# Kernel tuning notes

Measured on AMD Instinct MI355X. Metric: run time of the kernel, lower is better.

The kernel has to match this reference:

```python
import jax, jax.numpy as jnp
import numpy as np


def _gcn_conv(x, W, b, src, dst, dinv):
    # PyG GCNConv: linear transform, then symmetric-normalized aggregation, then bias
    n = x.shape[0]
    h = x @ W  # [N, out]
    norm = (dinv[src] * dinv[dst])[:, None]  # [E, 1]
    msg = h[src] * norm  # gather + scale, [E, out]
    out = jax.ops.segment_sum(msg, dst, num_segments=n)  # scatter-add
    return out + b


def setup_inputs() -> dict:
    key = jax.random.key(0)
    k1, k2, k3, k4 = jax.random.split(key, 4)
    N, E, F_IN, F_HID, F_OUT = 50000, 800000, 512, 256, 64
    x = jax.random.normal(k1, (N, F_IN), dtype=jnp.float32)
    edge_index = jax.random.randint(k2, (2, E), 0, N, dtype=jnp.int64)
    # Glorot-ish init for weights
    W1 = jax.random.normal(k3, (F_IN, F_HID), dtype=jnp.float32) * (1.0 / np.sqrt(F_IN))
    b1 = jnp.zeros((F_HID,), dtype=jnp.float32)
    W2 = jax.random.normal(k4, (F_HID, F_OUT), dtype=jnp.float32) * (1.0 / np.sqrt(F_HID))
    b2 = jnp.zeros((F_OUT,), dtype=jnp.float32)
    return {"x": x, "edge_index": edge_index, "W1": W1, "b1": b1, "W2": W2, "b2": b2}


def reference(x, edge_index, W1, b1, W2, b2):
    n = x.shape[0]
    # Add self loops (GCNConv default)
    loop = jnp.arange(n, dtype=edge_index.dtype)
    src = jnp.concatenate([edge_index[0], loop])
    dst = jnp.concatenate([edge_index[1], loop])
    # Symmetric normalization D^{-1/2} (A+I) D^{-1/2}
    deg = jax.ops.segment_sum(jnp.ones_like(dst, dtype=x.dtype), dst, num_segments=n)
    dinv = jnp.where(deg > 0, jax.lax.rsqrt(deg), 0.0)
    h = _gcn_conv(x, W1, b1, src, dst, dinv)
    h = jax.nn.relu(h)
    # Dropout(p=0.5) is identity in eval mode (deterministic reference)
    h = _gcn_conv(h, W2, b2, src, dst, dinv)
    return jax.nn.log_softmax(h, axis=1)
```

## Files before the change

### kernel.cpp

```cpp
#include <hip/hip_runtime.h>
#include <math.h>

#define F_IN  512
#define F_HID 256
#define F_OUT 64

typedef __attribute__((ext_vector_type(8))) short bf16x8;
typedef __attribute__((ext_vector_type(4))) short bf16x4;
typedef __attribute__((ext_vector_type(4))) float f32x4;

#define GLOBAL_AS __attribute__((address_space(1)))
#define LDS_AS    __attribute__((address_space(3)))

__device__ __forceinline__ void gload_lds16(const ushort* g, ushort* l) {
    __builtin_amdgcn_global_load_lds((const GLOBAL_AS uint32_t*)g,
                                     (LDS_AS uint32_t*)l, 16, 0, 0);
}

__device__ __forceinline__ ushort f2bf(float f) {
    union { float f; uint32_t u; } v; v.f = f;
    uint32_t r = (v.u + 0x7FFFu + ((v.u >> 16) & 1u)) >> 16;
    return (ushort)r;
}

__device__ __forceinline__ float bf2f(ushort u) {
    union { uint32_t u; float f; } v; v.u = ((uint32_t)u) << 16;
    return v.f;
}

__global__ void k_deg(const int* __restrict__ dst, int* __restrict__ deg, int E) {
    int e = blockIdx.x * 256 + threadIdx.x;
    if (e < E) atomicAdd(&deg[dst[e]], 1);
}

__global__ void k_scan1(const int* __restrict__ deg, int* __restrict__ offs,
                        int* __restrict__ bsums, float* __restrict__ dinv, int N) {
    __shared__ int s[256];
    int tid = threadIdx.x;
    int i = blockIdx.x * 256 + tid;
    int v = (i < N) ? deg[i] : 0;
    if (i < N) dinv[i] = rsqrtf((float)(v + 1));
    s[tid] = v; __syncthreads();
    for (int d = 1; d < 256; d <<= 1) {
        int t = (tid >= d) ? s[tid - d] : 0;
        __syncthreads();
        s[tid] += t;
        __syncthreads();
    }
    if (i < N) offs[i] = s[tid] - v;
    if (tid == 255) bsums[blockIdx.x] = s[255];
}

__global__ void k_scan2(int* __restrict__ bsums, int n) {
    __shared__ int s[256];
    int tid = threadIdx.x;
    int v = (tid < n) ? bsums[tid] : 0;
    s[tid] = v; __syncthreads();
    for (int d = 1; d < 256; d <<= 1) {
        int t = (tid >= d) ? s[tid - d] : 0;
        __syncthreads();
        s[tid] += t;
        __syncthreads();
    }
    if (tid < n) bsums[tid] = s[tid] - v;
}

__global__ void k_scan3(int* __restrict__ offs, const int* __restrict__ bsums,
                        int* __restrict__ cursor, int2* __restrict__ jw, int N, int E) {
    int i = blockIdx.x * 256 + threadIdx.x;
    if (i < N) {
        int o = offs[i] + bsums[i >> 8];
        offs[i] = o;
        cursor[i] = o;
    }
    if (i == 0) offs[N] = E;
    if (i < 16) jw[E + i] = make_int2(0, 0);
}

__global__ void k_fill(const int* __restrict__ src, const int* __restrict__ dst,
                       int* __restrict__ cursor, int2* __restrict__ jw,
                       const float* __restrict__ dinv, int E) {
    int e = blockIdx.x * 256 + threadIdx.x;
    if (e < E) {
        int s = src[e];
        int pos = atomicAdd(&cursor[dst[e]], 1);
        jw[pos] = make_int2(s, __float_as_int(dinv[s]));
    }
}

__global__ void k_tcast2(const float* __restrict__ W1, ushort* __restrict__ w1t,
                         const float* __restrict__ W2, ushort* __restrict__ w2t) {
    int idx = blockIdx.x * 256 + threadIdx.x;
    const int n1 = F_IN * F_HID;
    if (idx < n1) {
        int n = idx / F_IN, k = idx - n * F_IN;
        w1t[idx] = f2bf(W1[(size_t)k * F_HID + n]);
    } else {
        int t = idx - n1;
        if (t < F_HID * F_OUT) {
            int n = t / F_HID, k = t - n * F_HID;
            w2t[t] = f2bf(W2[(size_t)k * F_OUT + n]);
        }
    }
}

__global__ __launch_bounds__(256) void k_gemm1(
        const float* __restrict__ A, const ushort* __restrict__ Bt,
        ushort* __restrict__ C, int M) {
    constexpr int K = F_IN, Nc = F_HID, BM = 64, BN = 128, NT = K / 32;
    constexpr int ASTR = 36;
    __shared__ ushort As[2][BM * ASTR];
    __shared__ ushort Bs[2][BN * 32];
    const int tid  = threadIdx.x;
    const int wave = tid >> 6, lane = tid & 63;
    const int wr = wave & 1, wc = wave >> 1;
    const int brow = blockIdx.y * BM, bcol = blockIdx.x * BN;

    f32x4 acc[2][4];
    #pragma unroll
    for (int m = 0; m < 2; ++m)
        #pragma unroll
        for (int n = 0; n < 4; ++n) acc[m][n] = (f32x4){0.f, 0.f, 0.f, 0.f};

    const int arow = tid >> 2;
    const int akc  = (tid & 3) * 8;
    int agrow = brow + arow; if (agrow >= M) agrow = M - 1;
    const float4* ap = (const float4*)&A[(size_t)agrow * K + akc];
    const int csrc = (tid & 3) ^ ((tid >> 3) & 3);
    const ushort* bp0 = &Bt[(size_t)(bcol + (tid >> 2)) * K + csrc * 8];
    const ushort* bp1 = &Bt[(size_t)(bcol + 64 + (tid >> 2)) * K + csrc * 8];

    const int kqA = (lane >> 4) * 8;
    const int kqB = ((lane >> 4) ^ ((lane >> 1) & 3)) * 8;
    const int rA0 = wr * 32 + (lane & 15);
    const int rB0 = wc * 64 + (lane & 15);

    {
        float4 v0 = ap[0], v1 = ap[1];
        bf16x8 c0;
        c0[0] = (short)f2bf(v0.x); c0[1] = (short)f2bf(v0.y);
        c0[2] = (short)f2bf(v0.z); c0[3] = (short)f2bf(v0.w);
        c0[4] = (short)f2bf(v1.x); c0[5] = (short)f2bf(v1.y);
        c0[6] = (short)f2bf(v1.z); c0[7] = (short)f2bf(v1.w);
        *(bf16x8*)&As[0][arow * ASTR + akc] = c0;
        gload_lds16(bp0, &Bs[0][wave * 512]);
        gload_lds16(bp1, &Bs[0][2048 + wave * 512]);
    }
    __syncthreads();

    #pragma unroll
    for (int t = 0; t < NT; ++t) {
        const int b = t & 1;
        if (t + 1 < NT) {
            gload_lds16(bp0 + (t + 1) * 32, &Bs[b ^ 1][wave * 512]);
            gload_lds16(bp1 + (t + 1) * 32, &Bs[b ^ 1][2048 + wave * 512]);
            float4 v0 = ap[(t + 1) * 8], v1 = ap[(t + 1) * 8 + 1];
            bf16x8 c0;
            c0[0] = (short)f2bf(v0.x); c0[1] = (short)f2bf(v0.y);
            c0[2] = (short)f2bf(v0.z); c0[3] = (short)f2bf(v0.w);
            c0[4] = (short)f2bf(v1.x); c0[5] = (short)f2bf(v1.y);
            c0[6] = (short)f2bf(v1.z); c0[7] = (short)f2bf(v1.w);
            *(bf16x8*)&As[b ^ 1][arow * ASTR + akc] = c0;
        }
        bf16x8 af[2], bfr[4];
        #pragma unroll
        for (int m = 0; m < 2; ++m)
            af[m] = *(const bf16x8*)&As[b][(rA0 + m * 16) * ASTR + kqA];
        #pragma unroll
        for (int n = 0; n < 4; ++n)
            bfr[n] = *(const bf16x8*)&Bs[b][(rB0 + n * 16) * 32 + kqB];
        #pragma unroll
        for (int m = 0; m < 2; ++m)
            #pragma unroll
            for (int n = 0; n < 4; ++n)
                acc[m][n] = __builtin_amdgcn_mfma_f32_16x16x32_bf16(af[m], bfr[n], acc[m][n], 0, 0, 0);
        if (t + 1 < NT) __syncthreads();
    }

    const int crow0 = brow + wr * 32 + (lane >> 4) * 4;
    const int ccol0 = bcol + wc * 64 + (lane & 15);
    #pragma unroll
    for (int m = 0; m < 2; ++m)
        #pragma unroll
        for (int n = 0; n < 4; ++n)
            #pragma unroll
            for (int j = 0; j < 4; ++j) {
                int row = crow0 + m * 16 + j;
                if (row < M) C[(size_t)row * Nc + ccol0 + n * 16] = f2bf(acc[m][n][j]);
            }
}

template<int WR, int WC, int MR, int NR>
__global__ __launch_bounds__(256) void k_gemm_bf16(
        const ushort* __restrict__ A, const ushort* __restrict__ Bt,
        ushort* __restrict__ C, int M, int K, int Nc) {
    constexpr int BM = WR * MR * 16;
    constexpr int BN = WC * NR * 16;
    __shared__ ushort As[BM * 32];
    __shared__ ushort Bs[BN * 32];
    const int tid  = threadIdx.x;
    const int wave = tid >> 6, lane = tid & 63;
    const int wr = wave % WR, wc = wave / WR;
    const int brow = blockIdx.y * BM, bcol = blockIdx.x * BN;

    f32x4 acc[MR][NR];
    #pragma unroll
    for (int m = 0; m < MR; ++m)
        #pragma unroll
        for (int n = 0; n < NR; ++n) acc[m][n] = (f32x4){0.f, 0.f, 0.f, 0.f};

    const int srow = tid >> 2;
    const int scol = (tid & 3) * 8;
    const int kq  = (lane >> 4) * 8;
    const int rA0 = wr * MR * 16 + (lane & 15);
    const int rB0 = wc * NR * 16 + (lane & 15);

    for (int k0 = 0; k0 < K; k0 += 32) {
        #pragma unroll
        for (int l = 0; l < BM / 64; ++l) {
            int row = brow + l * 64 + srow;
            if (row >= M) row = M - 1;
            gload_lds16(&A[(size_t)row * K + k0 + scol], &As[l * 2048 + wave * 512]);
        }
        #pragma unroll
        for (int l = 0; l < BN / 64; ++l) {
            int row = bcol + l * 64 + srow;
            gload_lds16(&Bt[(size_t)row * K + k0 + scol], &Bs[l * 2048 + wave * 512]);
        }
        __syncthreads();
        bf16x8 af[MR], bfr[NR];
        #pragma unroll
        for (int m = 0; m < MR; ++m)
            af[m] = *(const bf16x8*)&As[(rA0 + m * 16) * 32 + kq];
        #pragma unroll
        for (int n = 0; n < NR; ++n)
            bfr[n] = *(const bf16x8*)&Bs[(rB0 + n * 16) * 32 + kq];
        #pragma unroll
        for (int m = 0; m < MR; ++m)
            #pragma unroll
            for (int n = 0; n < NR; ++n)
                acc[m][n] = __builtin_amdgcn_mfma_f32_16x16x32_bf16(af[m], bfr[n], acc[m][n], 0, 0, 0);
        __syncthreads();
    }

    const int crow0 = brow + wr * MR * 16 + (lane >> 4) * 4;
    const int ccol0 = bcol + wc * NR * 16 + (lane & 15);
    #pragma unroll
    for (int m = 0; m < MR; ++m)
        #pragma unroll
        for (int n = 0; n < NR; ++n)
            #pragma unroll
            for (int j = 0; j < 4; ++j) {
                int row = crow0 + m * 16 + j;
                if (row < M) C[(size_t)row * Nc + ccol0 + n * 16] = f2bf(acc[m][n][j]);
            }
}

__global__ __launch_bounds__(256) void k_agg1(
        const ushort* __restrict__ h, const int2* __restrict__ jw,
        const int* __restrict__ offs, const float* __restrict__ dinv,
        const float* __restrict__ bias, ushort* __restrict__ outm, int N) {
    int wave = threadIdx.x >> 6, lane = threadIdx.x & 63;
    int i = blockIdx.x * 4 + wave;
    if (i >= N) return;
    int g = lane & 31;
    int p = lane >> 5;
    float di = dinv[i];
    float acc[8];
    {
        bf16x8 hv = *(const bf16x8*)&h[(size_t)i * F_HID + g * 8];
        float w = (p == 0) ? di * di : 0.f;
        #pragma unroll
        for (int k = 0; k < 8; ++k) acc[k] = bf2f((ushort)hv[k]) * w;
    }
    int s = offs[i], e = offs[i + 1];
    for (int u = s; u < e; u += 12) {
        int2 a[6];
        #pragma unroll
        for (int q = 0; q < 6; ++q) a[q] = jw[u + 2 * q + p];
        bf16x8 hv[6];
        #pragma unroll
        for (int q = 0; q < 6; ++q)
            hv[q] = *(const bf16x8*)&h[(size_t)a[q].x * F_HID + g * 8];
        #pragma unroll
        for (int q = 0; q < 6; ++q) {
            float ww = (u + 2 * q + p < e) ? __int_as_float(a[q].y) * di : 0.f;
            #pragma unroll
            for (int k = 0; k < 8; ++k) acc[k] += bf2f((ushort)hv[q][k]) * ww;
        }
    }
    #pragma unroll
    for (int k = 0; k < 8; ++k) acc[k] += __shfl_xor(acc[k], 32, 64);
    if (p == 0) {
        float4 b0 = *(const float4*)&bias[g * 8];
        float4 b1 = *(const float4*)&bias[g * 8 + 4];
        bf16x8 o;
        o[0] = (short)f2bf(fmaxf(acc[0] + b0.x, 0.f));
        o[1] = (short)f2bf(fmaxf(acc[1] + b0.y, 0.f));
        o[2] = (short)f2bf(fmaxf(acc[2] + b0.z, 0.f));
        o[3] = (short)f2bf(fmaxf(acc[3] + b0.w, 0.f));
        o[4] = (short)f2bf(fmaxf(acc[4] + b1.x, 0.f));
        o[5] = (short)f2bf(fmaxf(acc[5] + b1.y, 0.f));
        o[6] = (short)f2bf(fmaxf(acc[6] + b1.z, 0.f));
        o[7] = (short)f2bf(fmaxf(acc[7] + b1.w, 0.f));
        *(bf16x8*)&outm[(size_t)i * F_HID + g * 8] = o;
    }
}

__global__ __launch_bounds__(256) void k_agg2(
        const ushort* __restrict__ h, const int2* __restrict__ jw,
        const int* __restrict__ offs, const float* __restrict__ dinv,
        const float* __restrict__ bias, float* __restrict__ outm, int N) {
    int wave = threadIdx.x >> 6, lane = threadIdx.x & 63;
    int i = blockIdx.x * 4 + wave;
    if (i >= N) return;
    float di = dinv[i];
    float acc = bf2f(h[(size_t)i * F_OUT + lane]) * di * di;
    int s = offs[i], e = offs[i + 1];
    for (int u = s; u < e; u += 8) {
        int2 a[8];
        #pragma unroll
        for (int q = 0; q < 8; ++q) a[q] = jw[u + q];
        float hv[8];
        #pragma unroll
        for (int q = 0; q < 8; ++q)
            hv[q] = bf2f(h[(size_t)a[q].x * F_OUT + lane]);
        #pragma unroll
        for (int q = 0; q < 8; ++q) {
            float ww = (u + q < e) ? __int_as_float(a[q].y) * di : 0.f;
            acc += hv[q] * ww;
        }
    }
    acc += bias[lane];
    float m = acc;
    #pragma unroll
    for (int o = 32; o >= 1; o >>= 1) m = fmaxf(m, __shfl_xor(m, o, 64));
    float ex = expf(acc - m);
    float ssum = ex;
    #pragma unroll
    for (int o = 32; o >= 1; o >>= 1) ssum += __shfl_xor(ssum, o, 64);
    outm[(size_t)i * F_OUT + lane] = acc - m - logf(ssum);
}

extern "C" void kernel_launch(void* const* d_in, const int* in_sizes, int n_in,
                              void* d_out, int out_size, void* d_ws, size_t ws_size,
                              hipStream_t stream) {
    const float* x  = (const float*)d_in[0];
    const int*   ei = (const int*)d_in[1];
    const float* W1 = (const float*)d_in[2];
    const float* b1 = (const float*)d_in[3];
    const float* W2 = (const float*)d_in[4];
    const float* b2 = (const float*)d_in[5];
    float* out = (float*)d_out;

    int N = in_sizes[0] / F_IN;
    int E = in_sizes[1] / 2;
    const int* src = ei;
    const int* dst = ei + E;

    ushort* w1t = (ushort*)d_ws;
    ushort* w2t = w1t + F_HID * F_IN;
    ushort* h1  = w2t + F_OUT * F_HID;
    ushort* a1  = h1 + (size_t)N * F_HID;
    int*    deg = (int*)(a1 + (size_t)N * F_HID);
    float*  dinv = (float*)(deg + N);
    int*    offs = (int*)(dinv + N);
    int*    cursor = offs + N + 1;
    int*    bsums  = cursor + N;
    int2*   jw = (int2*)(((uintptr_t)(bsums + 256) + 7) & ~(uintptr_t)7);
    ushort* h2 = h1;

    int nch = (N + 255) / 256;

    hipMemsetAsync(deg, 0, sizeof(int) * N, stream);
    k_deg <<<(E + 255) / 256, 256, 0, stream>>>(dst, deg, E);
    k_scan1<<<nch, 256, 0, stream>>>(deg, offs, bsums, dinv, N);
    k_scan2<<<1, 256, 0, stream>>>(bsums, nch);
    k_scan3<<<nch, 256, 0, stream>>>(offs, bsums, cursor, jw, N, E);
    k_fill<<<(E + 255) / 256, 256, 0, stream>>>(src, dst, cursor, jw, dinv, E);

    int ntc = F_IN * F_HID + F_HID * F_OUT;
    k_tcast2<<<(ntc + 255) / 256, 256, 0, stream>>>(W1, w1t, W2, w2t);

    k_gemm1<<<dim3(F_HID / 128, (N + 63) / 64), 256, 0, stream>>>(x, w1t, h1, N);
    k_agg1<<<(N + 3) / 4, 256, 0, stream>>>(h1, jw, offs, dinv, b1, a1, N);

    k_gemm_bf16<4, 1, 1, 4><<<dim3(1, (N + 63) / 64), 256, 0, stream>>>(
        a1, w2t, h2, N, F_HID, F_OUT);
    k_agg2<<<(N + 3) / 4, 256, 0, stream>>>(h2, jw, offs, dinv, b2, out, N);
}
```

Measured before the change: 254.1 us.

## Shrink gemm1 N-tile to 64 and prefetch fp32 A two steps ahead

Cuts the first GEMM's block tile from 64x128 to 64x64, which doubles the grid and halves per-wave accumulators. It also adds a register double buffer that loads the fp32 A tile two k-steps ahead before converting it to bf16 into LDS, hiding global load latency. The cost is that each fp32 x row is now read by four column blocks instead of two, doubling redundant A traffic, which may be absorbed by L2.

```diff
diff --git a/kernel.cpp b/kernel.cpp
--- a/kernel.cpp
+++ b/kernel.cpp
@@ -26,6 +26,15 @@
 __device__ __forceinline__ float bf2f(ushort u) {
     union { uint32_t u; float f; } v; v.u = ((uint32_t)u) << 16;
     return v.f;
+}
+
+__device__ __forceinline__ bf16x8 conv8(float4 a, float4 b) {
+    bf16x8 c;
+    c[0] = (short)f2bf(a.x); c[1] = (short)f2bf(a.y);
+    c[2] = (short)f2bf(a.z); c[3] = (short)f2bf(a.w);
+    c[4] = (short)f2bf(b.x); c[5] = (short)f2bf(b.y);
+    c[6] = (short)f2bf(b.z); c[7] = (short)f2bf(b.w);
+    return c;
 }
 
 __global__ void k_deg(const int* __restrict__ dst, int* __restrict__ deg, int E) {
@@ -107,7 +116,7 @@
 __global__ __launch_bounds__(256) void k_gemm1(
         const float* __restrict__ A, const ushort* __restrict__ Bt,
         ushort* __restrict__ C, int M) {
-    constexpr int K = F_IN, Nc = F_HID, BM = 64, BN = 128, NT = K / 32;
+    constexpr int K = F_IN, Nc = F_HID, BM = 64, BN = 64, NT = K / 32;
     constexpr int ASTR = 36;
     __shared__ ushort As[2][BM * ASTR];
     __shared__ ushort Bs[2][BN * 32];
@@ -116,73 +125,65 @@
     const int wr = wave & 1, wc = wave >> 1;
     const int brow = blockIdx.y * BM, bcol = blockIdx.x * BN;
 
-    f32x4 acc[2][4];
+    f32x4 acc[2][2];
     #pragma unroll
     for (int m = 0; m < 2; ++m)
         #pragma unroll
-        for (int n = 0; n < 4; ++n) acc[m][n] = (f32x4){0.f, 0.f, 0.f, 0.f};
+        for (int n = 0; n < 2; ++n) acc[m][n] = (f32x4){0.f, 0.f, 0.f, 0.f};
 
     const int arow = tid >> 2;
     const int akc  = (tid & 3) * 8;
     int agrow = brow + arow; if (agrow >= M) agrow = M - 1;
     const float4* ap = (const float4*)&A[(size_t)agrow * K + akc];
     const int csrc = (tid & 3) ^ ((tid >> 3) & 3);
-    const ushort* bp0 = &Bt[(size_t)(bcol + (tid >> 2)) * K + csrc * 8];
-    const ushort* bp1 = &Bt[(size_t)(bcol + 64 + (tid >> 2)) * K + csrc * 8];
+    const ushort* bp = &Bt[(size_t)(bcol + (tid >> 2)) * K + csrc * 8];
 
     const int kqA = (lane >> 4) * 8;
     const int kqB = ((lane >> 4) ^ ((lane >> 1) & 3)) * 8;
     const int rA0 = wr * 32 + (lane & 15);
-    const int rB0 = wc * 64 + (lane & 15);
-
-    {
-        float4 v0 = ap[0], v1 = ap[1];
-        bf16x8 c0;
-        c0[0] = (short)f2bf(v0.x); c0[1] = (short)f2bf(v0.y);
-        c0[2] = (short)f2bf(v0.z); c0[3] = (short)f2bf(v0.w);
-        c0[4] = (short)f2bf(v1.x); c0[5] = (short)f2bf(v1.y);
-        c0[6] = (short)f2bf(v1.z); c0[7] = (short)f2bf(v1.w);
-        *(bf16x8*)&As[0][arow * ASTR + akc] = c0;
-        gload_lds16(bp0, &Bs[0][wave * 512]);
-        gload_lds16(bp1, &Bs[0][2048 + wave * 512]);
-    }
+    const int rB0 = wc * 32 + (lane & 15);
+
+    float4 rg[2][2];
+
+    rg[0][0] = ap[0]; rg[0][1] = ap[1];
+    gload_lds16(bp, &Bs[0][wave * 512]);
+    *(bf16x8*)&As[0][arow * ASTR + akc] = conv8(rg[0][0], rg[0][1]);
+    rg[1][0] = ap[8]; rg[1][1] = ap[9];
     __syncthreads();
 
     #pragma unroll
     for (int t = 0; t < NT; ++t) {
         const int b = t & 1;
         if (t + 1 < NT) {
-            gload_lds16(bp0 + (t + 1) * 32, &Bs[b ^ 1][wave * 512]);
-            gload_lds16(bp1 + (t + 1) * 32, &Bs[b ^ 1][2048 + wave * 512]);
-            float4 v0 = ap[(t + 1) * 8], v1 = ap[(t + 1) * 8 + 1];
-            bf16x8 c0;
-            c0[0] = (short)f2bf(v0.x); c0[1] = (short)f2bf(v0.y);
-            c0[2] = (short)f2bf(v0.z); c0[3] = (short)f2bf(v0.w);
-            c0[4] = (short)f2bf(v1.x); c0[5] = (short)f2bf(v1.y);
-            c0[6] = (short)f2bf(v1.z); c0[7] = (short)f2bf(v1.w);
-            *(bf16x8*)&As[b ^ 1][arow * ASTR + akc] = c0;
-        }
-        bf16x8 af[2], bfr[4];
+            gload_lds16(bp + (t + 1) * 32, &Bs[b ^ 1][wave * 512]);
+            *(bf16x8*)&As[b ^ 1][arow * ASTR + akc] =
+                conv8(rg[(t + 1) & 1][0], rg[(t + 1) & 1][1]);
+        }
+        if (t + 2 < NT) {
+            rg[t & 1][0] = ap[(t + 2) * 8];
+            rg[t & 1][1] = ap[(t + 2) * 8 + 1];
+        }
+        bf16x8 af[2], bfr[2];
         #pragma unroll
         for (int m = 0; m < 2; ++m)
             af[m] = *(const bf16x8*)&As[b][(rA0 + m * 16) * ASTR + kqA];
         #pragma unroll
-        for (int n = 0; n < 4; ++n)
+        for (int n = 0; n < 2; ++n)
             bfr[n] = *(const bf16x8*)&Bs[b][(rB0 + n * 16) * 32 + kqB];
         #pragma unroll
         for (int m = 0; m < 2; ++m)
             #pragma unroll
-            for (int n = 0; n < 4; ++n)
+            for (int n = 0; n < 2; ++n)
                 acc[m][n] = __builtin_amdgcn_mfma_f32_16x16x32_bf16(af[m], bfr[n], acc[m][n], 0, 0, 0);
         if (t + 1 < NT) __syncthreads();
     }
 
     const int crow0 = brow + wr * 32 + (lane >> 4) * 4;
-    const int ccol0 = bcol + wc * 64 + (lane & 15);
+    const int ccol0 = bcol + wc * 32 + (lane & 15);
     #pragma unroll
     for (int m = 0; m < 2; ++m)
         #pragma unroll
-        for (int n = 0; n < 4; ++n)
+        for (int n = 0; n < 2; ++n)
             #pragma unroll
             for (int j = 0; j < 4; ++j) {
                 int row = crow0 + m * 16 + j;
@@ -382,7 +383,7 @@
     int ntc = F_IN * F_HID + F_HID * F_OUT;
     k_tcast2<<<(ntc + 255) / 256, 256, 0, stream>>>(W1, w1t, W2, w2t);
 
-    k_gemm1<<<dim3(F_HID / 128, (N + 63) / 64), 256, 0, stream>>>(x, w1t, h1, N);
+    k_gemm1<<<dim3(F_HID / 64, (N + 63) / 64), 256, 0, stream>>>(x, w1t, h1, N);
     k_agg1<<<(N + 3) / 4, 256, 0, stream>>>(h1, jw, offs, dinv, b1, a1, N);
 
     k_gemm_bf16<4, 1, 1, 4><<<dim3(1, (N + 63) / 64), 256, 0, stream>>>(
```

Result: slower. 270.9 us (+6.6%).
